# Optimization experiments

Hardware: AMD Instinct MI355X
Metric: run time of the kernel (lower is better)

The kernel has to match this reference:

```python
import jax, jax.numpy as jnp
import numpy as np

N_EMBD = 512
HEAD_SIZE = 64
T = 4096
B = 4


def setup_inputs() -> dict:
    key = jax.random.key(0)
    kx, kq, kk, kv = jax.random.split(key, 4)
    x = jax.random.normal(kx, (B, T, N_EMBD), dtype=jnp.float32)
    # torch nn.Linear(n_embd, head_size, bias=False): weight [head_size, n_embd];
    # stored here transposed as [n_embd, head_size] so projection is x @ W.
    s = 1.0 / np.sqrt(N_EMBD)
    Wq = jax.random.uniform(kq, (N_EMBD, HEAD_SIZE), jnp.float32, -s, s)
    Wk = jax.random.uniform(kk, (N_EMBD, HEAD_SIZE), jnp.float32, -s, s)
    Wv = jax.random.uniform(kv, (N_EMBD, HEAD_SIZE), jnp.float32, -s, s)
    return {"x": x, "Wq": Wq, "Wk": Wk, "Wv": Wv}


def reference(x, Wq, Wk, Wv):
    Bq, Tq, C = x.shape
    q = x @ Wq  # [B,T,H]
    k = x @ Wk  # [B,T,H]
    v = x @ Wv  # [B,T,H]
    # NOTE: original scales by C**-0.5 with C = n_embd (input dim), not head_size.
    wei = jnp.einsum('bqh,bkh->bqk', q, k) * (C ** -0.5)  # [B,T,T]
    causal = jnp.tril(jnp.ones((Tq, Tq), dtype=bool))
    wei = jnp.where(causal, wei, -jnp.inf)
    wei = jax.nn.softmax(wei, axis=-1)
    # dropout p=0.0 -> identity (eval-mode deterministic baseline)
    out = jnp.einsum('bqk,bkh->bqh', wei, v)  # [B,T,H]
    return out
```

## Files before the change

### kernel.cpp

```cpp
#include <hip/hip_runtime.h>
#include <hip/hip_bf16.h>
#include <math.h>

#define T_SEQ 4096
#define NBATCH 4
#define C_EMB 512
#define HEAD 64
#define CHUNK 8
#define EPB 288

typedef __attribute__((ext_vector_type(8))) short short8;
typedef __attribute__((ext_vector_type(4))) short short4v;
typedef __attribute__((ext_vector_type(4))) float f32x4;

#define C2 (0.044194173824159216f * 1.44269504088896340736f)

__device__ __forceinline__ unsigned short f2bf(float f) {
    union { float f; unsigned u; } v; v.f = f;
    unsigned u = v.u;
    u += 0x7FFF + ((u >> 16) & 1);
    return (unsigned short)(u >> 16);
}
__device__ __forceinline__ unsigned pk2bf(float a, float b) {
    __hip_bfloat162 h = __float22bfloat162_rn(make_float2(a, b));
    return *(unsigned*)&h;
}
__device__ __forceinline__ float bf2f(unsigned short u) {
    union { unsigned u; float f; } v; v.u = ((unsigned)u) << 16;
    return v.f;
}

__global__ __launch_bounds__(64) void wcvt_kernel(
    const float* __restrict__ Wq, const float* __restrict__ Wk,
    const float* __restrict__ Wv, unsigned short* __restrict__ wt)
{
    const int w = blockIdx.x >> 6;
    const int n = blockIdx.x & 63;
    const float* W = (w == 0) ? Wq : (w == 1) ? Wk : Wv;
    const int k0 = threadIdx.x * 8;
    unsigned short tmp[8];
#pragma unroll
    for (int i = 0; i < 8; ++i) tmp[i] = f2bf(W[(size_t)(k0 + i) * HEAD + n]);
    *(short8*)(wt + ((size_t)blockIdx.x) * C_EMB + k0) = *(short8*)tmp;
}

__global__ __launch_bounds__(512, 4) void proj_kernel(
    const float* __restrict__ x,
    const unsigned short* __restrict__ wt,
    unsigned short* __restrict__ qout,
    unsigned short* __restrict__ kout,
    unsigned short* __restrict__ vt)
{
    __shared__ unsigned short Wl[2][192][72];
    __shared__ unsigned short Xl[2][32][72];

    const int tid  = threadIdx.x;
    const int wave = tid >> 6;
    const int lane = tid & 63;
    const int l16  = lane & 15;
    const int quad = lane >> 4;
    const int row0 = blockIdx.x * 32;
    const int mq   = wave & 1;
    const int ng   = wave >> 1;

    const int wrow = tid >> 3;
    const int wsc  = (tid & 7) * 8;
    const bool xst = tid < 256;
    const int xrow = tid >> 3;
    const int xc8  = (tid & 7) * 8;

    f32x4 acc[3];
#pragma unroll
    for (int j = 0; j < 3; ++j) acc[j] = (f32x4){0.f, 0.f, 0.f, 0.f};

#pragma unroll
    for (int m = 0; m < 3; ++m) {
        int row = wrow + m * 64;
        *(short8*)&Wl[0][row][wsc] = *(const short8*)(wt + (size_t)row * C_EMB + wsc);
    }
    if (xst) {
        const float* xs = x + (size_t)(row0 + xrow) * C_EMB + xc8;
        float4 a = *(const float4*)(xs);
        float4 b = *(const float4*)(xs + 4);
        int4 ai = make_int4((int)pk2bf(a.x, a.y), (int)pk2bf(a.z, a.w),
                            (int)pk2bf(b.x, b.y), (int)pk2bf(b.z, b.w));
        *(short8*)&Xl[0][xrow][xc8] = *(short8*)&ai;
    }
    __syncthreads();

    for (int c = 0; c < 8; ++c) {
        const int bb = c & 1;
        if (c < 7) {
            const int nb = bb ^ 1;
            const int kc0 = (c + 1) * 64;
#pragma unroll
            for (int m = 0; m < 3; ++m) {
                int row = wrow + m * 64;
                *(short8*)&Wl[nb][row][wsc] =
                    *(const short8*)(wt + (size_t)row * C_EMB + kc0 + wsc);
            }
            if (xst) {
                const float* xs = x + (size_t)(row0 + xrow) * C_EMB + kc0 + xc8;
                float4 a = *(const float4*)(xs);
                float4 b = *(const float4*)(xs + 4);
                int4 ai = make_int4((int)pk2bf(a.x, a.y), (int)pk2bf(a.z, a.w),
                                    (int)pk2bf(b.x, b.y), (int)pk2bf(b.z, b.w));
                *(short8*)&Xl[nb][xrow][xc8] = *(short8*)&ai;
            }
        }

#pragma unroll
        for (int kc = 0; kc < 2; ++kc) {
            short8 a0 = *(const short8*)&Xl[bb][mq * 16 + l16][kc * 32 + quad * 8];
#pragma unroll
            for (int j = 0; j < 3; ++j) {
                const int ct = ng * 3 + j;
                short8 bfr = *(const short8*)&Wl[bb][ct * 16 + l16][kc * 32 + quad * 8];
                acc[j] = __builtin_amdgcn_mfma_f32_16x16x32_bf16(a0, bfr, acc[j], 0, 0, 0);
            }
        }
        __syncthreads();
    }

    unsigned short (*Vsh)[40] = (unsigned short (*)[40]) & Xl[0][0][0];
#pragma unroll
    for (int j = 0; j < 3; ++j) {
        const int ct = ng * 3 + j;
        const int m  = ct >> 2;
        const int n  = ct & 3;
#pragma unroll
        for (int r = 0; r < 4; ++r) {
            const int row = row0 + mq * 16 + quad * 4 + r;
            if (m == 0)
                qout[(size_t)row * HEAD + n * 16 + l16] = f2bf(acc[j][r] * C2);
            else if (m == 1)
                kout[(size_t)row * HEAD + n * 16 + l16] = f2bf(acc[j][r]);
            else
                Vsh[n * 16 + l16][mq * 16 + quad * 4 + r] = f2bf(acc[j][r]);
        }
    }
    __syncthreads();
    if (tid < 256) {
        int h  = tid >> 2;
        int tc = (tid & 3) * 8;
        int b  = row0 >> 12;
        int t0 = row0 & (T_SEQ - 1);
        unsigned short* dst = vt + ((size_t)(b * HEAD + h)) * T_SEQ + t0 + tc;
        *(short8*)dst = *(const short8*)&Vsh[h][tc];
    }
}

__device__ __forceinline__ void stage_v(unsigned short (*Vbuf)[72], int sr, int phiA,
                                        short8 v0, short8 v1) {
    *(short4v*)&Vbuf[sr][phiA]      = __builtin_shufflevector(v0, v0, 0, 1, 2, 3);
    *(short4v*)&Vbuf[sr][phiA + 8]  = __builtin_shufflevector(v0, v0, 4, 5, 6, 7);
    *(short4v*)&Vbuf[sr][phiA + 16] = __builtin_shufflevector(v1, v1, 0, 1, 2, 3);
    *(short4v*)&Vbuf[sr][phiA + 24] = __builtin_shufflevector(v1, v1, 4, 5, 6, 7);
}

__global__ __launch_bounds__(256) void attn1_kernel(
    const unsigned short* __restrict__ qb,
    const unsigned short* __restrict__ kb,
    const unsigned short* __restrict__ vt,
    unsigned short* __restrict__ po,
    float* __restrict__ pl)
{
    __shared__ unsigned short Ks[2][64][72];
    __shared__ unsigned short Vs[2][64][72];

    const int tid  = threadIdx.x;
    const int wave = tid >> 6;
    const int lane = tid & 63;
    const int l16  = lane & 15;
    const int quad = lane >> 4;

    const int b = blockIdx.x / EPB;
    const int e = blockIdx.x % EPB;
    int g = 0;
#pragma unroll
    for (int gg = 1; gg < 8; ++gg) if (e >= 4 * gg * (gg + 1)) g = gg;
    const int rem = e - 4 * g * (g + 1);
    const int t   = rem / (g + 1);
    const int c   = rem - t * (g + 1);
    const int qt  = 8 * g + t;

    const size_t base = (size_t)b * T_SEQ;
    const int qrow = qt * 64 + wave * 16 + l16;
    short8 aq0 = *(const short8*)(qb + (base + qrow) * HEAD + quad * 8);
    short8 aq1 = *(const short8*)(qb + (base + qrow) * HEAD + 32 + quad * 8);

    float lacc = 0.f;
    f32x4 o[4];
#pragma unroll
    for (int n = 0; n < 4; ++n) o[n] = (f32x4){0.f, 0.f, 0.f, 0.f};

    const int kt0 = c * CHUNK;
    const int np  = min(CHUNK, qt + 1 - kt0);

    const int sr   = tid >> 2;
    const int sc   = (tid & 3) * 16;
    const int phiA = (sc & 32) + ((sc & 16) >> 2);

    short8 kra, krb, vra, vrb;
    {
        const int kbase = kt0 * 64;
        const unsigned short* ksrc = kb + (base + kbase + sr) * HEAD + sc;
        const unsigned short* vsrc = vt + ((size_t)(b * HEAD + sr)) * T_SEQ + kbase + sc;
        kra = *(const short8*)(ksrc);     krb = *(const short8*)(ksrc + 8);
        vra = *(const short8*)(vsrc);     vrb = *(const short8*)(vsrc + 8);
    }
    *(short8*)&Ks[0][sr][sc]     = kra;  *(short8*)&Ks[0][sr][sc + 8] = krb;
    stage_v(Vs[0], sr, phiA, vra, vrb);

    for (int p = 0; p < np; ++p) {
        const int cur = p & 1;
        const int kbase = (kt0 + p) * 64;
        __syncthreads();

        if (p + 1 < np) {
            const int nb = kbase + 64;
            const unsigned short* ksrc = kb + (base + nb + sr) * HEAD + sc;
            const unsigned short* vsrc = vt + ((size_t)(b * HEAD + sr)) * T_SEQ + nb + sc;
            kra = *(const short8*)(ksrc);  krb = *(const short8*)(ksrc + 8);
            vra = *(const short8*)(vsrc);  vrb = *(const short8*)(vsrc + 8);
        }

        f32x4 s[4];
#pragma unroll
        for (int n = 0; n < 4; ++n) {
            short8 bk0 = *(const short8*)&Ks[cur][n * 16 + l16][quad * 8];
            short8 bk1 = *(const short8*)&Ks[cur][n * 16 + l16][32 + quad * 8];
            f32x4 accS = (f32x4){0.f, 0.f, 0.f, 0.f};
            accS = __builtin_amdgcn_mfma_f32_16x16x32_bf16(bk0, aq0, accS, 0, 0, 0);
            accS = __builtin_amdgcn_mfma_f32_16x16x32_bf16(bk1, aq1, accS, 0, 0, 0);
            s[n] = accS;
        }

#pragma unroll
        for (int n = 0; n < 4; ++n)
#pragma unroll
            for (int r = 0; r < 4; ++r)
                s[n][r] = __builtin_amdgcn_exp2f(s[n][r]);

        if (kbase + 64 > qt * 64) {
            const int cb = kbase + quad * 4;
#pragma unroll
            for (int n = 0; n < 4; ++n)
#pragma unroll
                for (int r = 0; r < 4; ++r)
                    if (cb + n * 16 + r > qrow) s[n][r] = 0.f;
        }

#pragma unroll
        for (int n = 0; n < 4; ++n)
            lacc += (s[n][0] + s[n][1]) + (s[n][2] + s[n][3]);

#pragma unroll
        for (int st = 0; st < 2; ++st) {
            int4 ai = make_int4(
                (int)pk2bf(s[2 * st][0],     s[2 * st][1]),
                (int)pk2bf(s[2 * st][2],     s[2 * st][3]),
                (int)pk2bf(s[2 * st + 1][0], s[2 * st + 1][1]),
                (int)pk2bf(s[2 * st + 1][2], s[2 * st + 1][3]));
            short8 af = *(short8*)&ai;
#pragma unroll
            for (int n = 0; n < 4; ++n) {
                short8 bv = *(const short8*)&Vs[cur][n * 16 + l16][32 * st + quad * 8];
                o[n] = __builtin_amdgcn_mfma_f32_16x16x32_bf16(af, bv, o[n], 0, 0, 0);
            }
        }

        if (p + 1 < np) {
            const int nxt = cur ^ 1;
            *(short8*)&Ks[nxt][sr][sc]     = kra;  *(short8*)&Ks[nxt][sr][sc + 8] = krb;
            stage_v(Vs[nxt], sr, phiA, vra, vrb);
        }
    }

    lacc += __shfl_xor(lacc, 16);
    lacc += __shfl_xor(lacc, 32);

    const int pid = blockIdx.x;
#pragma unroll
    for (int n = 0; n < 4; ++n)
#pragma unroll
        for (int r = 0; r < 4; ++r) {
            int lr = wave * 16 + quad * 4 + r;
            po[(size_t)pid * 4096 + lr * 64 + n * 16 + l16] = f2bf(o[n][r]);
        }
    if (quad == 0)
        pl[pid * 64 + wave * 16 + l16] = lacc;
}

__global__ __launch_bounds__(256) void combine_kernel(
    const unsigned short* __restrict__ po, const float* __restrict__ pl,
    float* __restrict__ out)
{
    const int gth = blockIdx.x * 256 + threadIdx.x;
    const int h8  = gth & 7;
    const int row = gth >> 3;
    const int lr  = row & 63;
    const int qt  = (row >> 6) & 63;
    const int b   = row >> 12;
    const int nc  = (qt >> 3) + 1;
    const int g   = qt >> 3;
    const int rem = qt & 7;
    const int e0  = 4 * g * (g + 1) + rem * (g + 1);
    const int pid0 = b * EPB + e0;

    float l = 0.f;
    float acc[8];
#pragma unroll
    for (int i = 0; i < 8; ++i) acc[i] = 0.f;
    for (int cc = 0; cc < nc; ++cc) {
        l += pl[(pid0 + cc) * 64 + lr];
        short8 p8 = *(const short8*)(po + (size_t)(pid0 + cc) * 4096 + lr * 64 + h8 * 8);
#pragma unroll
        for (int i = 0; i < 8; ++i) acc[i] += bf2f((unsigned short)p8[i]);
    }
    float inv = 1.f / l;
    float4 r0 = make_float4(acc[0] * inv, acc[1] * inv, acc[2] * inv, acc[3] * inv);
    float4 r1 = make_float4(acc[4] * inv, acc[5] * inv, acc[6] * inv, acc[7] * inv);
    float* dst = out + (size_t)gth * 8;
    *(float4*)dst       = r0;
    *(float4*)(dst + 4) = r1;
}

extern "C" void kernel_launch(void* const* d_in, const int* in_sizes, int n_in,
                              void* d_out, int out_size, void* d_ws, size_t ws_size,
                              hipStream_t stream) {
    const float* x  = (const float*)d_in[0];
    const float* Wq = (const float*)d_in[1];
    const float* Wk = (const float*)d_in[2];
    const float* Wv = (const float*)d_in[3];
    float* out = (float*)d_out;

    char* ws = (char*)d_ws;
    unsigned short* qb = (unsigned short*)(ws);
    unsigned short* kb = (unsigned short*)(ws + (2u << 20));
    unsigned short* vt = (unsigned short*)(ws + (4u << 20));
    unsigned short* wt = (unsigned short*)(ws + (6u << 20));
    float* pl = (float*)(ws + (6u << 20) + 196608);
    unsigned short* po = (unsigned short*)(ws + (6u << 20) + 196608 + 294912);

    wcvt_kernel<<<dim3(192), dim3(64), 0, stream>>>(Wq, Wk, Wv, wt);
    proj_kernel<<<dim3(512), dim3(512), 0, stream>>>(x, wt, qb, kb, vt);
    attn1_kernel<<<dim3(NBATCH * EPB), dim3(256), 0, stream>>>(qb, kb, vt, po, pl);
    combine_kernel<<<dim3(512), dim3(256), 0, stream>>>(po, pl, out);
}
```

Measured before the change: 112.9 us.

## Pre-swizzle weights into MFMA fragment order and load via direct global-to-LDS

The weight conversion kernel now writes bf16 weights in a layout matching the MFMA B-fragment order per 64-wide K chunk. The projection kernel then streams each chunk into LDS with global_load_lds (bypassing registers) and reads fragments with contiguous per-lane 16-byte accesses. This is meant to cut register traffic and LDS bank conflicts in the projection stage. The projection is a small part of the pipeline, so the overall effect is bounded, and the async LDS load relies on the existing barriers for ordering.

```diff
diff --git a/kernel.cpp b/kernel.cpp
--- a/kernel.cpp
+++ b/kernel.cpp
@@ -30,28 +30,38 @@
     return v.f;
 }
 
+#define GLD_LDS16(gp, lp)                                                     \
+    __builtin_amdgcn_global_load_lds(                                         \
+        (const __attribute__((address_space(1))) void*)(gp),                  \
+        (__attribute__((address_space(3))) void*)(lp), 16, 0, 0)
+
 __global__ __launch_bounds__(64) void wcvt_kernel(
     const float* __restrict__ Wq, const float* __restrict__ Wk,
-    const float* __restrict__ Wv, unsigned short* __restrict__ wt)
+    const float* __restrict__ Wv, unsigned short* __restrict__ wt2)
 {
-    const int w = blockIdx.x >> 6;
-    const int n = blockIdx.x & 63;
-    const float* W = (w == 0) ? Wq : (w == 1) ? Wk : Wv;
-    const int k0 = threadIdx.x * 8;
+    const int gid  = blockIdx.x * 64 + threadIdx.x;
+    const int lane = gid & 63;
+    int rest = gid >> 6;
+    const int kc   = rest & 1; rest >>= 1;
+    const int tile = rest % 12;
+    const int c    = rest / 12;
+    const float* W = (tile < 4) ? Wq : (tile < 8) ? Wk : Wv;
+    const int n  = (tile & 3) * 16 + (lane & 15);
+    const int k0 = c * 64 + kc * 32 + (lane >> 4) * 8;
     unsigned short tmp[8];
 #pragma unroll
     for (int i = 0; i < 8; ++i) tmp[i] = f2bf(W[(size_t)(k0 + i) * HEAD + n]);
-    *(short8*)(wt + ((size_t)blockIdx.x) * C_EMB + k0) = *(short8*)tmp;
+    *(short8*)(wt2 + (size_t)gid * 8) = *(short8*)tmp;
 }
 
 __global__ __launch_bounds__(512, 4) void proj_kernel(
     const float* __restrict__ x,
-    const unsigned short* __restrict__ wt,
+    const unsigned short* __restrict__ wt2,
     unsigned short* __restrict__ qout,
     unsigned short* __restrict__ kout,
     unsigned short* __restrict__ vt)
 {
-    __shared__ unsigned short Wl[2][192][72];
+    __shared__ unsigned short Wl[2][12288];
     __shared__ unsigned short Xl[2][32][72];
 
     const int tid  = threadIdx.x;
@@ -63,8 +73,6 @@
     const int mq   = wave & 1;
     const int ng   = wave >> 1;
 
-    const int wrow = tid >> 3;
-    const int wsc  = (tid & 7) * 8;
     const bool xst = tid < 256;
     const int xrow = tid >> 3;
     const int xc8  = (tid & 7) * 8;
@@ -74,10 +82,9 @@
     for (int j = 0; j < 3; ++j) acc[j] = (f32x4){0.f, 0.f, 0.f, 0.f};
 
 #pragma unroll
-    for (int m = 0; m < 3; ++m) {
-        int row = wrow + m * 64;
-        *(short8*)&Wl[0][row][wsc] = *(const short8*)(wt + (size_t)row * C_EMB + wsc);
-    }
+    for (int m = 0; m < 3; ++m)
+        GLD_LDS16(wt2 + (size_t)(m * 4096 + wave * 512 + lane * 8),
+                  &Wl[0][m * 4096 + wave * 512]);
     if (xst) {
         const float* xs = x + (size_t)(row0 + xrow) * C_EMB + xc8;
         float4 a = *(const float4*)(xs);
@@ -92,15 +99,13 @@
         const int bb = c & 1;
         if (c < 7) {
             const int nb = bb ^ 1;
-            const int kc0 = (c + 1) * 64;
-#pragma unroll
-            for (int m = 0; m < 3; ++m) {
-                int row = wrow + m * 64;
-                *(short8*)&Wl[nb][row][wsc] =
-                    *(const short8*)(wt + (size_t)row * C_EMB + kc0 + wsc);
-            }
+            const size_t g0 = (size_t)(c + 1) * 12288;
+#pragma unroll
+            for (int m = 0; m < 3; ++m)
+                GLD_LDS16(wt2 + g0 + (size_t)(m * 4096 + wave * 512 + lane * 8),
+                          &Wl[nb][m * 4096 + wave * 512]);
             if (xst) {
-                const float* xs = x + (size_t)(row0 + xrow) * C_EMB + kc0 + xc8;
+                const float* xs = x + (size_t)(row0 + xrow) * C_EMB + (c + 1) * 64 + xc8;
                 float4 a = *(const float4*)(xs);
                 float4 b = *(const float4*)(xs + 4);
                 int4 ai = make_int4((int)pk2bf(a.x, a.y), (int)pk2bf(a.z, a.w),
@@ -115,7 +120,7 @@
 #pragma unroll
             for (int j = 0; j < 3; ++j) {
                 const int ct = ng * 3 + j;
-                short8 bfr = *(const short8*)&Wl[bb][ct * 16 + l16][kc * 32 + quad * 8];
+                short8 bfr = *(const short8*)&Wl[bb][(ct * 128 + kc * 64 + lane) * 8];
                 acc[j] = __builtin_amdgcn_mfma_f32_16x16x32_bf16(a0, bfr, acc[j], 0, 0, 0);
             }
         }
@@ -339,12 +344,12 @@
     unsigned short* qb = (unsigned short*)(ws);
     unsigned short* kb = (unsigned short*)(ws + (2u << 20));
     unsigned short* vt = (unsigned short*)(ws + (4u << 20));
-    unsigned short* wt = (unsigned short*)(ws + (6u << 20));
+    unsigned short* wt2 = (unsigned short*)(ws + (6u << 20));
     float* pl = (float*)(ws + (6u << 20) + 196608);
     unsigned short* po = (unsigned short*)(ws + (6u << 20) + 196608 + 294912);
 
-    wcvt_kernel<<<dim3(192), dim3(64), 0, stream>>>(Wq, Wk, Wv, wt);
-    proj_kernel<<<dim3(512), dim3(512), 0, stream>>>(x, wt, qb, kb, vt);
+    wcvt_kernel<<<dim3(192), dim3(64), 0, stream>>>(Wq, Wk, Wv, wt2);
+    proj_kernel<<<dim3(512), dim3(512), 0, stream>>>(x, wt2, qb, kb, vt);
     attn1_kernel<<<dim3(NBATCH * EPB), dim3(256), 0, stream>>>(qb, kb, vt, po, pl);
     combine_kernel<<<dim3(512), dim3(256), 0, stream>>>(po, pl, out);
 }
```

New measurement: 110.4 us. 2.2% less time.
